# Performance work log

Hardware: AMD Instinct MI355X
Metric: run time of the kernel (lower is better)

Reference implementation:

```python
import jax, jax.numpy as jnp
import numpy as np


def setup_inputs() -> dict:
    key = jax.random.key(0)
    B, H, C, T = 8, 8, 64, 2048
    qkv = jax.random.normal(key, (B, 3 * H * C, T), dtype=jnp.float32)
    return {"qkv": qkv, "n_heads": H}


def reference(qkv, n_heads):
    # qkv: (B, 3*H*C, T)
    bs, width, length = qkv.shape
    ch = width // (3 * n_heads)
    q, k, v = jnp.split(qkv, 3, axis=1)          # each (B, H*C, T)
    scale = ch ** (-0.25)
    q = (q * scale).reshape(bs * n_heads, ch, length)
    k = (k * scale).reshape(bs * n_heads, ch, length)
    v = v.reshape(bs * n_heads, ch, length)
    # weight[b, t, s] = sum_c q[b,c,t] * k[b,c,s]
    weight = jnp.einsum('bct,bcs->bts', q, k)
    weight = jax.nn.softmax(weight.astype(jnp.float32), axis=-1).astype(qkv.dtype)
    out = jnp.einsum('bts,bcs->bct', weight, v)   # (B*H, C, T)
    return out.reshape(bs, n_heads * ch, length)
```

## Files before the change

kernel.cpp:

```cpp
#include <hip/hip_runtime.h>

typedef __bf16 bf16x4 __attribute__((ext_vector_type(4)));
typedef __bf16 bf16x8 __attribute__((ext_vector_type(8)));
typedef float floatx4 __attribute__((ext_vector_type(4)));
typedef float floatx16 __attribute__((ext_vector_type(16)));

#define T_SEQ 2048
#define TTILE 512
#define STILE 64
#define LOG2E_SCALE 0.18033688011112042f

__device__ __forceinline__ unsigned pack_bf16_pair(float a, float b) {
    unsigned ua = __builtin_bit_cast(unsigned, a) + 0x8000u;
    unsigned ub = __builtin_bit_cast(unsigned, b) + 0x8000u;
    return __builtin_amdgcn_perm(ub, ua, 0x07060302u);
}
__device__ __forceinline__ unsigned short bf16_bits(float a) {
    return (unsigned short)((__builtin_bit_cast(unsigned, a) + 0x8000u) >> 16);
}

__global__ __launch_bounds__(512, 2) void attn_fused(
    const float* __restrict__ qkv, float* __restrict__ out)
{
    __shared__ __align__(16) __bf16 Kt[2][STILE][72];
    __shared__ __align__(16) __bf16 Vs[2][64][72];

    const int tid  = threadIdx.x;
    const int lane = tid & 63;
    const int wave = tid >> 6;
    const int l31  = lane & 31;
    const int g    = lane >> 5;

    const int bh = blockIdx.y;
    const int b = bh >> 3, head = bh & 7;
    const size_t in_base = ((size_t)b * 1536 + head * 64) * T_SEQ;
    const float* Qg = qkv + in_base;
    const float* Kg = qkv + in_base + (size_t)512 * T_SEQ;
    const float* Vg = qkv + in_base + (size_t)1024 * T_SEQ;

    const int tcol0 = blockIdx.x * TTILE + wave * 64 + l31;
    const int tcol1 = tcol0 + 32;

    bf16x8 qf[2][4];
    #pragma unroll
    for (int kb = 0; kb < 4; ++kb)
        #pragma unroll
        for (int j = 0; j < 8; ++j) {
            size_t rowoff = (size_t)(kb * 16 + g * 8 + j) * T_SEQ;
            qf[0][kb][j] = (__bf16)(Qg[rowoff + tcol0] * LOG2E_SCALE);
            qf[1][kb][j] = (__bf16)(Qg[rowoff + tcol1] * LOG2E_SCALE);
        }

    floatx16 zf;
    #pragma unroll
    for (int r = 0; r < 16; ++r) zf[r] = 0.0f;

    union U4 { unsigned u[4]; bf16x8 v; };
    U4 one0, one1;
    {
        unsigned p0 = (l31 == 0) ? 0x3F803F80u : 0u;
        unsigned p1 = (l31 == 1) ? 0x3F803F80u : 0u;
        one0.u[0] = p0; one0.u[1] = p0; one0.u[2] = p0; one0.u[3] = p0;
        one1.u[0] = p1; one1.u[1] = p1; one1.u[2] = p1; one1.u[3] = p1;
    }

    floatx16 Oa[2][2];
    floatx16 La = zf;
    Oa[0][0] = zf; Oa[0][1] = zf; Oa[1][0] = zf; Oa[1][1] = zf;

    int cc[2], ss[2];
    size_t goff[2];
    #pragma unroll
    for (int r = 0; r < 2; ++r) {
        int i = tid + r * 512;
        cc[r] = i >> 4;
        ss[r] = (i & 15) * 4;
        goff[r] = (size_t)cc[r] * T_SEQ + ss[r];
    }
    const int ph = (tid >> 1) & 3;

    floatx4 kr[2], vr[2];
    #pragma unroll
    for (int r = 0; r < 2; ++r) {
        kr[r] = *(const floatx4*)(Kg + goff[r]);
        vr[r] = *(const floatx4*)(Vg + goff[r]);
    }
    #pragma unroll
    for (int r = 0; r < 2; ++r) {
        int c = cc[r], s4 = ss[r];
        #pragma unroll
        for (int k = 0; k < 4; ++k) {
            int d = (k + ph) & 3;
            *(unsigned short*)&Kt[0][s4 + d][c] = bf16_bits(kr[r][d]);
        }
        union { unsigned u[2]; bf16x4 v; } vb;
        vb.u[0] = pack_bf16_pair(vr[r][0], vr[r][1]);
        vb.u[1] = pack_bf16_pair(vr[r][2], vr[r][3]);
        *(bf16x4*)&Vs[0][c][s4] = vb.v;
    }

    for (int it = 0; it < T_SEQ / STILE; ++it) {
        const int rb = it & 1;
        const int s_next = (it + 1) * STILE;
        const bool pref = (s_next < T_SEQ);

        __syncthreads();

        if (pref) {
            #pragma unroll
            for (int r = 0; r < 2; ++r) {
                kr[r] = *(const floatx4*)(Kg + goff[r] + s_next);
                vr[r] = *(const floatx4*)(Vg + goff[r] + s_next);
            }
        }

        const __bf16 (*KtR)[72] = Kt[rb];
        const __bf16 (*VsR)[72] = Vs[rb];

        bf16x8 pf[2][4];
        #pragma unroll
        for (int ms = 0; ms < 2; ++ms) {
            floatx16 Sa0, Sa1;
            {
                bf16x8 kf = *(const bf16x8*)&KtR[ms * 32 + l31][g * 8];
                Sa0 = __builtin_amdgcn_mfma_f32_32x32x16_bf16(kf, qf[0][0], zf, 0, 0, 0);
                Sa1 = __builtin_amdgcn_mfma_f32_32x32x16_bf16(kf, qf[1][0], zf, 0, 0, 0);
            }
            #pragma unroll
            for (int kb = 1; kb < 4; ++kb) {
                bf16x8 kf = *(const bf16x8*)&KtR[ms * 32 + l31][kb * 16 + g * 8];
                Sa0 = __builtin_amdgcn_mfma_f32_32x32x16_bf16(kf, qf[0][kb], Sa0, 0, 0, 0);
                Sa1 = __builtin_amdgcn_mfma_f32_32x32x16_bf16(kf, qf[1][kb], Sa1, 0, 0, 0);
            }
            #pragma unroll
            for (int tt = 0; tt < 2; ++tt) {
                const floatx16& Sa = tt ? Sa1 : Sa0;
                float p[16];
                #pragma unroll
                for (int r = 0; r < 16; ++r)
                    p[r] = __builtin_amdgcn_exp2f(Sa[r]);
                unsigned d[8];
                #pragma unroll
                for (int q = 0; q < 8; ++q) d[q] = pack_bf16_pair(p[2 * q], p[2 * q + 1]);
                #pragma unroll
                for (int kb = 0; kb < 2; ++kb) {
                    unsigned d0 = d[4 * kb + 0], d1 = d[4 * kb + 1];
                    unsigned d2 = d[4 * kb + 2], d3 = d[4 * kb + 3];
                    unsigned sendA = g ? d0 : d2;
                    unsigned sendB = g ? d1 : d3;
                    unsigned recvA = (unsigned)__shfl_xor((int)sendA, 32);
                    unsigned recvB = (unsigned)__shfl_xor((int)sendB, 32);
                    union { unsigned u[4]; bf16x8 v; } fu;
                    fu.u[0] = g ? recvA : d0;
                    fu.u[1] = g ? recvB : d1;
                    fu.u[2] = g ? d2    : recvA;
                    fu.u[3] = g ? d3    : recvB;
                    pf[tt][ms * 2 + kb] = fu.v;
                }
            }
        }

        #pragma unroll
        for (int mc = 0; mc < 2; ++mc)
            #pragma unroll
            for (int kb2 = 0; kb2 < 4; ++kb2) {
                bf16x8 vf = *(const bf16x8*)&VsR[mc * 32 + l31][kb2 * 16 + g * 8];
                Oa[0][mc] = __builtin_amdgcn_mfma_f32_32x32x16_bf16(vf, pf[0][kb2], Oa[0][mc], 0, 0, 0);
                Oa[1][mc] = __builtin_amdgcn_mfma_f32_32x32x16_bf16(vf, pf[1][kb2], Oa[1][mc], 0, 0, 0);
            }
        #pragma unroll
        for (int kb2 = 0; kb2 < 4; ++kb2) {
            La = __builtin_amdgcn_mfma_f32_32x32x16_bf16(one0.v, pf[0][kb2], La, 0, 0, 0);
            La = __builtin_amdgcn_mfma_f32_32x32x16_bf16(one1.v, pf[1][kb2], La, 0, 0, 0);
        }

        if (pref) {
            __bf16 (*KtW)[72] = Kt[rb ^ 1];
            __bf16 (*VsW)[72] = Vs[rb ^ 1];
            #pragma unroll
            for (int r = 0; r < 2; ++r) {
                int c = cc[r], s4 = ss[r];
                #pragma unroll
                for (int k = 0; k < 4; ++k) {
                    int d = (k + ph) & 3;
                    *(unsigned short*)&KtW[s4 + d][c] = bf16_bits(kr[r][d]);
                }
                union { unsigned u[2]; bf16x4 v; } vb;
                vb.u[0] = pack_bf16_pair(vr[r][0], vr[r][1]);
                vb.u[1] = pack_bf16_pair(vr[r][2], vr[r][3]);
                *(bf16x4*)&VsW[c][s4] = vb.v;
            }
        }
    }

    float d0 = La[0], d1 = La[1];
    float rl0 = 1.0f / (d0 + __shfl_xor(d0, 32));
    float rl1 = 1.0f / (d1 + __shfl_xor(d1, 32));

    const size_t out_base = ((size_t)b * 512 + head * 64) * T_SEQ;
    #pragma unroll
    for (int mc = 0; mc < 2; ++mc)
        #pragma unroll
        for (int r = 0; r < 16; ++r) {
            int c = mc * 32 + (r & 3) + 8 * (r >> 2) + 4 * g;
            size_t row = out_base + (size_t)c * T_SEQ;
            out[row + tcol0] = Oa[0][mc][r] * rl0;
            out[row + tcol1] = Oa[1][mc][r] * rl1;
        }
}

extern "C" void kernel_launch(void* const* d_in, const int* in_sizes, int n_in,
                              void* d_out, int out_size, void* d_ws, size_t ws_size,
                              hipStream_t stream) {
    const float* qkv = (const float*)d_in[0];
    float* out = (float*)d_out;
    dim3 grid(T_SEQ / TTILE, 64);
    attn_fused<<<grid, dim3(512), 0, stream>>>(qkv, out);
}
```

Baseline: 210.3 us.

## Use hardware bf16 pack and permlane32 swap, interleave PV MFMAs per sub-tile

Replaces the software bf16 round-and-perm with the v_cvt_pk_bf16_f32 instruction and swaps the half-wave data exchange from ds-based shfl_xor and selects to the gfx950 permlane32_swap builtin. It also moves the PV and row-sum MFMAs inside the per-32-row S loop, so each half of P is consumed right after it is produced. The aim is to shorten the exp/pack/exchange path, lower register pressure from holding all of P, and let softmax VALU work overlap with MFMA. The hardware convert uses round-to-nearest-even rather than the previous round-half-up, which changes rounding slightly.

New measurement: 200.9 us. 1.05x faster.

```diff
diff --git a/kernel.cpp b/kernel.cpp
--- a/kernel.cpp
+++ b/kernel.cpp
@@ -4,16 +4,17 @@
 typedef __bf16 bf16x8 __attribute__((ext_vector_type(8)));
 typedef float floatx4 __attribute__((ext_vector_type(4)));
 typedef float floatx16 __attribute__((ext_vector_type(16)));
+typedef unsigned uintx2 __attribute__((ext_vector_type(2)));
 
 #define T_SEQ 2048
 #define TTILE 512
 #define STILE 64
 #define LOG2E_SCALE 0.18033688011112042f
 
-__device__ __forceinline__ unsigned pack_bf16_pair(float a, float b) {
-    unsigned ua = __builtin_bit_cast(unsigned, a) + 0x8000u;
-    unsigned ub = __builtin_bit_cast(unsigned, b) + 0x8000u;
-    return __builtin_amdgcn_perm(ub, ua, 0x07060302u);
+__device__ __forceinline__ unsigned cvt_pk_bf16(float a, float b) {
+    unsigned r;
+    asm("v_cvt_pk_bf16_f32 %0, %1, %2" : "=v"(r) : "v"(a), "v"(b));
+    return r;
 }
 __device__ __forceinline__ unsigned short bf16_bits(float a) {
     return (unsigned short)((__builtin_bit_cast(unsigned, a) + 0x8000u) >> 16);
@@ -94,8 +95,8 @@
             *(unsigned short*)&Kt[0][s4 + d][c] = bf16_bits(kr[r][d]);
         }
         union { unsigned u[2]; bf16x4 v; } vb;
-        vb.u[0] = pack_bf16_pair(vr[r][0], vr[r][1]);
-        vb.u[1] = pack_bf16_pair(vr[r][2], vr[r][3]);
+        vb.u[0] = cvt_pk_bf16(vr[r][0], vr[r][1]);
+        vb.u[1] = cvt_pk_bf16(vr[r][2], vr[r][3]);
         *(bf16x4*)&Vs[0][c][s4] = vb.v;
     }
 
@@ -117,7 +118,6 @@
         const __bf16 (*KtR)[72] = Kt[rb];
         const __bf16 (*VsR)[72] = Vs[rb];
 
-        bf16x8 pf[2][4];
         #pragma unroll
         for (int ms = 0; ms < 2; ++ms) {
             floatx16 Sa0, Sa1;
@@ -132,6 +132,8 @@
                 Sa0 = __builtin_amdgcn_mfma_f32_32x32x16_bf16(kf, qf[0][kb], Sa0, 0, 0, 0);
                 Sa1 = __builtin_amdgcn_mfma_f32_32x32x16_bf16(kf, qf[1][kb], Sa1, 0, 0, 0);
             }
+
+            bf16x8 pf[2][2];
             #pragma unroll
             for (int tt = 0; tt < 2; ++tt) {
                 const floatx16& Sa = tt ? Sa1 : Sa0;
@@ -141,37 +143,34 @@
                     p[r] = __builtin_amdgcn_exp2f(Sa[r]);
                 unsigned d[8];
                 #pragma unroll
-                for (int q = 0; q < 8; ++q) d[q] = pack_bf16_pair(p[2 * q], p[2 * q + 1]);
+                for (int q = 0; q < 8; ++q)
+                    d[q] = cvt_pk_bf16(p[2 * q], p[2 * q + 1]);
                 #pragma unroll
                 for (int kb = 0; kb < 2; ++kb) {
-                    unsigned d0 = d[4 * kb + 0], d1 = d[4 * kb + 1];
-                    unsigned d2 = d[4 * kb + 2], d3 = d[4 * kb + 3];
-                    unsigned sendA = g ? d0 : d2;
-                    unsigned sendB = g ? d1 : d3;
-                    unsigned recvA = (unsigned)__shfl_xor((int)sendA, 32);
-                    unsigned recvB = (unsigned)__shfl_xor((int)sendB, 32);
-                    union { unsigned u[4]; bf16x8 v; } fu;
-                    fu.u[0] = g ? recvA : d0;
-                    fu.u[1] = g ? recvB : d1;
-                    fu.u[2] = g ? d2    : recvA;
-                    fu.u[3] = g ? d3    : recvB;
-                    pf[tt][ms * 2 + kb] = fu.v;
+                    uintx2 s02 = __builtin_amdgcn_permlane32_swap(
+                        d[4 * kb + 0], d[4 * kb + 2], false, false);
+                    uintx2 s13 = __builtin_amdgcn_permlane32_swap(
+                        d[4 * kb + 1], d[4 * kb + 3], false, false);
+                    U4 fu;
+                    fu.u[0] = s02[0]; fu.u[1] = s13[0];
+                    fu.u[2] = s02[1]; fu.u[3] = s13[1];
+                    pf[tt][kb] = fu.v;
                 }
             }
-        }
-
-        #pragma unroll
-        for (int mc = 0; mc < 2; ++mc)
-            #pragma unroll
-            for (int kb2 = 0; kb2 < 4; ++kb2) {
-                bf16x8 vf = *(const bf16x8*)&VsR[mc * 32 + l31][kb2 * 16 + g * 8];
-                Oa[0][mc] = __builtin_amdgcn_mfma_f32_32x32x16_bf16(vf, pf[0][kb2], Oa[0][mc], 0, 0, 0);
-                Oa[1][mc] = __builtin_amdgcn_mfma_f32_32x32x16_bf16(vf, pf[1][kb2], Oa[1][mc], 0, 0, 0);
-            }
-        #pragma unroll
-        for (int kb2 = 0; kb2 < 4; ++kb2) {
-            La = __builtin_amdgcn_mfma_f32_32x32x16_bf16(one0.v, pf[0][kb2], La, 0, 0, 0);
-            La = __builtin_amdgcn_mfma_f32_32x32x16_bf16(one1.v, pf[1][kb2], La, 0, 0, 0);
+
+            #pragma unroll
+            for (int mc = 0; mc < 2; ++mc)
+                #pragma unroll
+                for (int kb = 0; kb < 2; ++kb) {
+                    bf16x8 vf = *(const bf16x8*)&VsR[mc * 32 + l31][(ms * 2 + kb) * 16 + g * 8];
+                    Oa[0][mc] = __builtin_amdgcn_mfma_f32_32x32x16_bf16(vf, pf[0][kb], Oa[0][mc], 0, 0, 0);
+                    Oa[1][mc] = __builtin_amdgcn_mfma_f32_32x32x16_bf16(vf, pf[1][kb], Oa[1][mc], 0, 0, 0);
+                }
+            #pragma unroll
+            for (int kb = 0; kb < 2; ++kb) {
+                La = __builtin_amdgcn_mfma_f32_32x32x16_bf16(one0.v, pf[0][kb], La, 0, 0, 0);
+                La = __builtin_amdgcn_mfma_f32_32x32x16_bf16(one1.v, pf[1][kb], La, 0, 0, 0);
+            }
         }
 
         if (pref) {
@@ -186,8 +185,8 @@
                     *(unsigned short*)&KtW[s4 + d][c] = bf16_bits(kr[r][d]);
                 }
                 union { unsigned u[2]; bf16x4 v; } vb;
-                vb.u[0] = pack_bf16_pair(vr[r][0], vr[r][1]);
-                vb.u[1] = pack_bf16_pair(vr[r][2], vr[r][3]);
+                vb.u[0] = cvt_pk_bf16(vr[r][0], vr[r][1]);
+                vb.u[1] = cvt_pk_bf16(vr[r][2], vr[r][3]);
                 *(bf16x4*)&VsW[c][s4] = vb.v;
             }
         }
```
